# Performance work log

Measured on AMD Instinct MI355X. Metric: run time of the kernel, lower is better.

Reference implementation:

```python
import jax, jax.numpy as jnp
import numpy as np

TREE_DEPTH = 3
N_LEAVES = 2 ** TREE_DEPTH
TEMPERATURE = 1.0
N_HEADS = 16
SOFTPLUS_SHIFT = 0.5413


def _build_path_indices(n_leaves, tree_depth):
    pi = np.zeros((n_leaves, tree_depth), dtype=np.int32)
    pd = np.zeros((n_leaves, tree_depth), dtype=np.float32)
    for leaf in range(n_leaves):
        node = 0
        for d in range(tree_depth):
            pi[leaf, d] = node
            bit = (leaf >> (tree_depth - 1 - d)) & 1
            pd[leaf, d] = 1.0 - bit
            node = 2 * node + 1 + bit
    return pi, pd

PATH_IDX, PATH_DIR = _build_path_indices(N_LEAVES, TREE_DEPTH)


def setup_inputs() -> dict:
    key = jax.random.key(0)
    ks = jax.random.split(key, 8)
    B, S, D = 4, 1024, 1024
    T, N, L, H = 12, 7, 8, 3
    return {
        "x": jax.random.normal(ks[0], (B, S, D), jnp.float32),
        "decision_weights": jax.random.normal(ks[1], (T, N, D), jnp.float32) * 0.1,
        "decision_biases": jnp.zeros((T, N), jnp.float32),
        "node_temperature_logits": jnp.zeros((T, N), jnp.float32),
        "gate_w": jax.random.normal(ks[2], (D, T), jnp.float32) * (1.0 / np.sqrt(D)),
        "gate_b": jnp.zeros((T,), jnp.float32),
        "leaf_outputs": jax.random.normal(ks[3], (H, T, L, D), jnp.float32) * np.sqrt(2.0 / (L + D)),
        "out_w": jax.random.normal(ks[4], (D, D), jnp.float32) * (1.0 / np.sqrt(D)),
        "out_b": jnp.zeros((D,), jnp.float32),
    }


def _forest_qkv(x, dw, db, ntl, gate_w, gate_b, leaf_out):
    # routing: [B,S,T,n_internal]
    decisions = jnp.einsum('bsd,tnd->bstn', x, dw) + db
    node_temps = TEMPERATURE * jax.nn.softplus(ntl + SOFTPLUS_SHIFT)
    decisions = jax.nn.sigmoid(decisions / node_temps)
    # gather nodes along each root-to-leaf path: [B,S,T,L,depth]
    relevant = decisions[..., PATH_IDX]
    probs_per_level = PATH_DIR * relevant + (1.0 - PATH_DIR) * (1.0 - relevant)
    leaf_probs = jnp.prod(probs_per_level, axis=-1)  # [B,S,T,L]
    weights = jax.nn.softmax(x @ gate_w + gate_b, axis=-1)  # [B,S,T]
    # fused per-tree mix + gate combine (same math as per_tree->outputs)
    qkv = jnp.einsum('bstl,bst,htld->hbsd', leaf_probs, weights, leaf_out)
    return qkv[0], qkv[1], qkv[2]


def reference(x, decision_weights, decision_biases, node_temperature_logits,
              gate_w, gate_b, leaf_outputs, out_w, out_b):
    B, S, D = x.shape
    dh = D // N_HEADS
    q, k, v = _forest_qkv(x, decision_weights, decision_biases,
                          node_temperature_logits, gate_w, gate_b, leaf_outputs)
    q = q.reshape(B, S, N_HEADS, dh)
    k = k.reshape(B, S, N_HEADS, dh)
    v = v.reshape(B, S, N_HEADS, dh)
    scale = 1.0 / np.sqrt(dh)
    scores = jnp.einsum('bqhd,bkhd->bhqk', q, k) * scale
    causal = np.tril(np.ones((S, S), dtype=bool))
    scores = jnp.where(causal, scores, jnp.float32(-1e9))
    attn = jax.nn.softmax(scores, axis=-1)
    ctx = jnp.einsum('bhqk,bkhd->bqhd', attn, v).reshape(B, S, D)
    return ctx @ out_w + out_b
```

## Files before the change

kernel.cpp:

```cpp
#include <hip/hip_runtime.h>
#include <hip/hip_bf16.h>
#include <math.h>

#define TOKS 4096

typedef __attribute__((ext_vector_type(4))) float    f32x4;
typedef __attribute__((ext_vector_type(8))) short    short8;
typedef __attribute__((ext_vector_type(4))) unsigned short ushort4v;
typedef unsigned short ushort;

__device__ __forceinline__ ushort f2b(float f) {
    unsigned int b = __float_as_uint(f);
    b += 0x7fff + ((b >> 16) & 1);
    return (ushort)(b >> 16);
}

__global__ __launch_bounds__(256) void wb_kernel(
    const float* __restrict__ dw,
    const float* __restrict__ gate_w,
    ushort* __restrict__ Wb)
{
    const int i = blockIdx.x * 256 + threadIdx.x;
    const int row = i >> 7, k0 = (i & 127) * 8;
    short8 o;
    if (row < 84) {
        float4 a0 = *(const float4*)&dw[(size_t)row*1024 + k0];
        float4 a1 = *(const float4*)&dw[(size_t)row*1024 + k0 + 4];
        o[0]=(short)f2b(a0.x); o[1]=(short)f2b(a0.y); o[2]=(short)f2b(a0.z); o[3]=(short)f2b(a0.w);
        o[4]=(short)f2b(a1.x); o[5]=(short)f2b(a1.y); o[6]=(short)f2b(a1.z); o[7]=(short)f2b(a1.w);
    } else {
        const int t = row - 84;
        #pragma unroll
        for (int j = 0; j < 8; ++j) o[j] = (short)f2b(gate_w[(size_t)(k0+j)*12 + t]);
    }
    *(short8*)&Wb[(size_t)row*1024 + k0] = o;
}

__global__ __launch_bounds__(64) void route2_kernel(
    const float* __restrict__ x,
    const ushort* __restrict__ Wb,
    const float* __restrict__ db,
    const float* __restrict__ ntl,
    const float* __restrict__ gate_b,
    ushort* __restrict__ coeffb)
{
    const int tok0 = blockIdx.x * 16;
    const int lane = threadIdx.x;
    const int lq = lane & 15, lg = lane >> 4;
    __shared__ float lgt[16][97];

    f32x4 acc[6];
    #pragma unroll
    for (int n = 0; n < 6; ++n) acc[n] = (f32x4){0.f,0.f,0.f,0.f};

    for (int k0 = 0; k0 < 1024; k0 += 32) {
        float4 a0 = *(const float4*)&x[(size_t)(tok0 + lq)*1024 + k0 + lg*8];
        float4 a1 = *(const float4*)&x[(size_t)(tok0 + lq)*1024 + k0 + lg*8 + 4];
        short8 af;
        af[0]=(short)f2b(a0.x); af[1]=(short)f2b(a0.y); af[2]=(short)f2b(a0.z); af[3]=(short)f2b(a0.w);
        af[4]=(short)f2b(a1.x); af[5]=(short)f2b(a1.y); af[6]=(short)f2b(a1.z); af[7]=(short)f2b(a1.w);
        #pragma unroll
        for (int n = 0; n < 6; ++n) {
            short8 bf_ = *(const short8*)&Wb[(size_t)(n*16 + lq)*1024 + k0 + lg*8];
            acc[n] = __builtin_amdgcn_mfma_f32_16x16x32_bf16(af, bf_, acc[n], 0, 0, 0);
        }
    }

    #pragma unroll
    for (int n = 0; n < 6; ++n)
        #pragma unroll
        for (int r = 0; r < 4; ++r)
            lgt[lg*4 + r][n*16 + lq] = acc[n][r];
    __builtin_amdgcn_wave_barrier();

    const int tok = lane >> 2;
    #pragma unroll
    for (int tj = 0; tj < 3; ++tj) {
        const int t = (lane & 3)*3 + tj;
        float dec[7];
        #pragma unroll
        for (int n = 0; n < 7; ++n) {
            float tempv = log1pf(expf(ntl[t*7+n] + 0.5413f));
            float v = (lgt[tok][t*7+n] + db[t*7+n]) / tempv;
            dec[n] = 1.f / (1.f + expf(-v));
        }
        float g[12], gmax = -3e38f;
        #pragma unroll
        for (int tt = 0; tt < 12; ++tt) {
            g[tt] = lgt[tok][84+tt] + gate_b[tt];
            gmax = fmaxf(gmax, g[tt]);
        }
        float gsum = 0.f;
        #pragma unroll
        for (int tt = 0; tt < 12; ++tt) gsum += expf(g[tt]-gmax);
        const float wgt = expf(g[t]-gmax) / gsum;
        short8 co;
        #pragma unroll
        for (int l = 0; l < 8; ++l) {
            float p = wgt; int node = 0;
            #pragma unroll
            for (int dpt = 0; dpt < 3; ++dpt) {
                int bit = (l >> (2-dpt)) & 1;
                float r = dec[node];
                p *= bit ? (1.f - r) : r;
                node = 2*node + 1 + bit;
            }
            co[l] = (short)f2b(p);
        }
        *(short8*)&coeffb[(size_t)(tok0 + tok)*96 + t*8] = co;
    }
}

__global__ __launch_bounds__(256) void lt_kernel(
    const float* __restrict__ leaf, ushort* __restrict__ leafT)
{
    __shared__ float t[96][65];
    const int d0 = blockIdx.x * 64, h = blockIdx.y;
    const int tid = threadIdx.x;
    for (int i = tid; i < 96*16; i += 256) {
        int k = i >> 4, c4 = i & 15;
        *(float4*)&t[k][c4*4] = *(const float4*)&leaf[(size_t)(h*96 + k)*1024 + d0 + c4*4];
    }
    __syncthreads();
    const int d = tid >> 2, kq = (tid & 3) * 24;
    #pragma unroll
    for (int base = 0; base < 24; base += 8) {
        short8 o;
        #pragma unroll
        for (int j = 0; j < 8; ++j) o[j] = (short)f2b(t[kq+base+j][d]);
        *(short8*)&leafT[(size_t)(h*1024 + d0 + d)*96 + kq + base] = o;
    }
}

__global__ __launch_bounds__(256) void mix_kernel(
    const ushort* __restrict__ coeffb,
    const ushort* __restrict__ leafT,
    ushort* __restrict__ qkvb,
    ushort* __restrict__ vT)
{
    const int bt = blockIdx.x;
    const int bd = blockIdx.y;
    const int tid = threadIdx.x, w = tid >> 6, lane = tid & 63;
    const int lq = lane & 15, lg = lane >> 4;
    const int tok0 = bt*64 + w*16;
    const int c0 = bd*128;
    const int pl = c0 >> 10;
    const int d0 = c0 & 1023;

    f32x4 acc[8];
    #pragma unroll
    for (int n = 0; n < 8; ++n) acc[n] = (f32x4){0.f,0.f,0.f,0.f};

    #pragma unroll
    for (int ks = 0; ks < 3; ++ks) {
        const int k0 = ks*32;
        short8 bfrag = *(const short8*)&coeffb[(tok0 + lq)*96 + k0 + lg*8];
        #pragma unroll
        for (int n = 0; n < 8; ++n) {
            short8 afrag = *(const short8*)&leafT[(size_t)(pl*1024 + d0 + n*16 + lq)*96 + k0 + lg*8];
            acc[n] = __builtin_amdgcn_mfma_f32_16x16x32_bf16(afrag, bfrag, acc[n], 0, 0, 0);
        }
    }

    const int tok = tok0 + lq;
    if (pl < 2) {
        #pragma unroll
        for (int n = 0; n < 8; ++n) {
            const int d = d0 + n*16 + lg*4;
            ushort4v u;
            u[0]=f2b(acc[n][0]); u[1]=f2b(acc[n][1]);
            u[2]=f2b(acc[n][2]); u[3]=f2b(acc[n][3]);
            *(ushort4v*)&qkvb[(size_t)pl*TOKS*1024 + (size_t)tok*1024 + d] = u;
        }
    } else {
        const int b = tok >> 10, seq = tok & 1023;
        #pragma unroll
        for (int n = 0; n < 8; ++n) {
            #pragma unroll
            for (int r = 0; r < 4; ++r) {
                const int d = d0 + n*16 + lg*4 + r;
                const int head = d >> 6, dh = d & 63;
                vT[((size_t)((b*16+head)*64 + dh))*1024 + seq] = f2b(acc[n][r]);
            }
        }
    }
}

__global__ __launch_bounds__(256) void wtrans_kernel(
    const float* __restrict__ w, ushort* __restrict__ wT)
{
    __shared__ float t[64][65];
    const int n0 = blockIdx.x * 64, k0 = blockIdx.y * 64;
    const int tid = threadIdx.x;
    const int r = tid >> 2, c16 = (tid & 3) * 16;
    #pragma unroll
    for (int j = 0; j < 16; j += 4)
        *(float4*)&t[r][c16+j] = *(const float4*)&w[(size_t)(k0+r)*1024 + n0 + c16 + j];
    __syncthreads();
    short8 o0, o1;
    #pragma unroll
    for (int j = 0; j < 8; ++j) o0[j] = (short)f2b(t[c16+j][r]);
    #pragma unroll
    for (int j = 0; j < 8; ++j) o1[j] = (short)f2b(t[c16+8+j][r]);
    *(short8*)&wT[(size_t)(n0+r)*1024 + k0 + c16]     = o0;
    *(short8*)&wT[(size_t)(n0+r)*1024 + k0 + c16 + 8] = o1;
}

__global__ __launch_bounds__(64) void attn_kernel(
    const ushort* __restrict__ qk,
    const ushort* __restrict__ vT,
    ushort* __restrict__ ctxb)
{
    const int id = blockIdx.x;
    const int bh = id & 63;
    const int qt = 63 - (id >> 6);
    const int b = bh >> 4, h = bh & 15;
    const int lane = threadIdx.x;
    const int lq = lane & 15, lg = lane >> 4;
    __shared__ unsigned int pTu[128][13];

    const size_t plane = (size_t)TOKS*1024;
    const int tokq = b*1024 + qt*16 + lq;
    short8 aq[2];
    aq[0] = *(const short8*)&qk[(size_t)tokq*1024 + h*64 + lg*8];
    aq[1] = *(const short8*)&qk[(size_t)tokq*1024 + h*64 + 32 + lg*8];

    f32x4 o[4];
    #pragma unroll
    for (int n = 0; n < 4; ++n) o[n] = (f32x4){0.f,0.f,0.f,0.f};
    float m[4] = {-3e38f,-3e38f,-3e38f,-3e38f};
    float l[4] = {0.f,0.f,0.f,0.f};

    const ushort* Kp  = qk + plane;
    const ushort* vTp = vT + (size_t)bh*64*1024;
    const int nt = (qt >> 3) + 1;

    for (int t = 0; t < nt; ++t) {
        const int tk0 = b*1024 + t*128;
        f32x4 s[8];
        #pragma unroll
        for (int n = 0; n < 8; ++n) s[n] = (f32x4){0.f,0.f,0.f,0.f};
        #pragma unroll
        for (int kk = 0; kk < 2; ++kk)
            #pragma unroll
            for (int n = 0; n < 8; ++n) {
                short8 bk = *(const short8*)&Kp[(size_t)(tk0 + n*16 + lq)*1024 + h*64 + kk*32 + lg*8];
                s[n] = __builtin_amdgcn_mfma_f32_16x16x32_bf16(aq[kk], bk, s[n], 0, 0, 0);
            }

        const bool diag = (t == nt-1);
        if (diag) {
            #pragma unroll
            for (int n = 0; n < 8; ++n)
                #pragma unroll
                for (int r = 0; r < 4; ++r) {
                    float v = s[n][r] * 0.125f;
                    if (t*128 + n*16 + lq > qt*16 + lg*4 + r) v = -1e9f;
                    s[n][r] = v;
                }
        } else {
            #pragma unroll
            for (int n = 0; n < 8; ++n)
                #pragma unroll
                for (int r = 0; r < 4; ++r) s[n][r] *= 0.125f;
        }

        #pragma unroll
        for (int r = 0; r < 4; ++r) {
            float rm = fmaxf(fmaxf(fmaxf(s[0][r], s[1][r]), fmaxf(s[2][r], s[3][r])),
                             fmaxf(fmaxf(s[4][r], s[5][r]), fmaxf(s[6][r], s[7][r])));
            rm = fmaxf(rm, __shfl_xor(rm, 1));
            rm = fmaxf(rm, __shfl_xor(rm, 2));
            rm = fmaxf(rm, __shfl_xor(rm, 4));
            rm = fmaxf(rm, __shfl_xor(rm, 8));
            float mnew = fmaxf(m[r], rm);
            float corr = __expf(m[r] - mnew);
            float ps = 0.f;
            #pragma unroll
            for (int n = 0; n < 8; ++n) {
                float p = __expf(s[n][r] - mnew);
                s[n][r] = p; ps += p;
            }
            ps += __shfl_xor(ps, 1);
            ps += __shfl_xor(ps, 2);
            ps += __shfl_xor(ps, 4);
            ps += __shfl_xor(ps, 8);
            l[r] = l[r]*corr + ps;
            m[r] = mnew;
            o[0][r] *= corr; o[1][r] *= corr; o[2][r] *= corr; o[3][r] *= corr;
        }

        #pragma unroll
        for (int n = 0; n < 8; ++n) {
            unsigned int lo = (unsigned int)f2b(s[n][0]) | ((unsigned int)f2b(s[n][1]) << 16);
            unsigned int hi = (unsigned int)f2b(s[n][2]) | ((unsigned int)f2b(s[n][3]) << 16);
            pTu[n*16 + lq][lg*2]     = lo;
            pTu[n*16 + lq][lg*2 + 1] = hi;
        }
        __builtin_amdgcn_wave_barrier();

        short8 pa[4];
        #pragma unroll
        for (int kk = 0; kk < 4; ++kk)
            #pragma unroll
            for (int j = 0; j < 8; ++j) {
                unsigned int u = pTu[kk*32 + lg*8 + j][lq >> 1];
                pa[kk][j] = (short)(ushort)(u >> ((lq & 1) * 16));
            }
        __builtin_amdgcn_wave_barrier();

        #pragma unroll
        for (int kk = 0; kk < 4; ++kk)
            #pragma unroll
            for (int n = 0; n < 4; ++n) {
                short8 bv = *(const short8*)&vTp[(size_t)(n*16 + lq)*1024 + t*128 + kk*32 + lg*8];
                o[n] = __builtin_amdgcn_mfma_f32_16x16x32_bf16(pa[kk], bv, o[n], 0, 0, 0);
            }
    }

    #pragma unroll
    for (int r = 0; r < 4; ++r) {
        float inv = 1.f / l[r];
        int row = b*1024 + qt*16 + lg*4 + r;
        #pragma unroll
        for (int n = 0; n < 4; ++n)
            ctxb[(size_t)row*1024 + h*64 + n*16 + lq] = f2b(o[n][r] * inv);
    }
}

__global__ __launch_bounds__(256) void proj_kernel(
    const ushort* __restrict__ A,
    const ushort* __restrict__ Bt,
    const float* __restrict__ bias,
    float* __restrict__ out)
{
    const int bn = blockIdx.x, bm = blockIdx.y;
    const int tid = threadIdx.x, w = tid >> 6, lane = tid & 63;
    const int wm = w >> 1, wn = w & 1;
    const int lq = lane & 15, lg = lane >> 4;
    const int row0 = bm*128 + wm*64;
    const int col0 = bn*64 + wn*32;

    f32x4 acc[4][2];
    #pragma unroll
    for (int i = 0; i < 4; ++i)
        #pragma unroll
        for (int j = 0; j < 2; ++j) acc[i][j] = (f32x4){0.f,0.f,0.f,0.f};

    for (int k0 = 0; k0 < 1024; k0 += 32) {
        short8 a[4], bfr[2];
        #pragma unroll
        for (int i = 0; i < 4; ++i)
            a[i] = *(const short8*)&A[(size_t)(row0 + i*16 + lq)*1024 + k0 + lg*8];
        #pragma unroll
        for (int j = 0; j < 2; ++j)
            bfr[j] = *(const short8*)&Bt[(size_t)(col0 + j*16 + lq)*1024 + k0 + lg*8];
        #pragma unroll
        for (int i = 0; i < 4; ++i)
            #pragma unroll
            for (int j = 0; j < 2; ++j)
                acc[i][j] = __builtin_amdgcn_mfma_f32_16x16x32_bf16(a[i], bfr[j], acc[i][j], 0, 0, 0);
    }

    #pragma unroll
    for (int i = 0; i < 4; ++i)
        #pragma unroll
        for (int j = 0; j < 2; ++j) {
            int col = col0 + j*16 + lq;
            float bb = bias[col];
            #pragma unroll
            for (int r = 0; r < 4; ++r)
                out[(size_t)(row0 + i*16 + lg*4 + r)*1024 + col] = acc[i][j][r] + bb;
        }
}

extern "C" void kernel_launch(void* const* d_in, const int* in_sizes, int n_in,
                              void* d_out, int out_size, void* d_ws, size_t ws_size,
                              hipStream_t stream) {
    (void)in_sizes; (void)n_in; (void)out_size; (void)ws_size;
    const float* x      = (const float*)d_in[0];
    const float* dw     = (const float*)d_in[1];
    const float* db     = (const float*)d_in[2];
    const float* ntl    = (const float*)d_in[3];
    const float* gate_w = (const float*)d_in[4];
    const float* gate_b = (const float*)d_in[5];
    const float* leaf   = (const float*)d_in[6];
    const float* out_w  = (const float*)d_in[7];
    const float* out_b  = (const float*)d_in[8];
    float* out = (float*)d_out;

    ushort* coeffb = (ushort*)d_ws;
    ushort* Wb     = (ushort*)((char*)d_ws + ((size_t)1u  << 20));
    ushort* qkvb   = (ushort*)((char*)d_ws + ((size_t)2u  << 20));
    ushort* vT     = (ushort*)((char*)d_ws + ((size_t)20u << 20));
    ushort* ctxb   = (ushort*)((char*)d_ws + ((size_t)30u << 20));
    ushort* wT     = (ushort*)((char*)d_ws + ((size_t)40u << 20));
    ushort* leafT  = (ushort*)((char*)d_ws + ((size_t)44u << 20));

    hipLaunchKernelGGL(wb_kernel,      dim3(48),      dim3(256), 0, stream,
                       dw, gate_w, Wb);
    hipLaunchKernelGGL(lt_kernel,      dim3(16, 3),   dim3(256), 0, stream,
                       leaf, leafT);
    hipLaunchKernelGGL(wtrans_kernel,  dim3(16, 16),  dim3(256), 0, stream,
                       out_w, wT);
    hipLaunchKernelGGL(route2_kernel,  dim3(256),     dim3(64),  0, stream,
                       x, Wb, db, ntl, gate_b, coeffb);
    hipLaunchKernelGGL(mix_kernel,     dim3(64, 24),  dim3(256), 0, stream,
                       coeffb, leafT, qkvb, vT);
    hipLaunchKernelGGL(attn_kernel,    dim3(4096),    dim3(64),  0, stream,
                       qkvb, vT, ctxb);
    hipLaunchKernelGGL(proj_kernel,    dim3(16, 32),  dim3(256), 0, stream,
                       ctxb, wT, out_b, out);
}
```

Measured before the change: 290.0 us.

## Split routing GEMM K dimension across eight waves with shared-memory reduction

```diff
diff --git a/kernel.cpp b/kernel.cpp
--- a/kernel.cpp
+++ b/kernel.cpp
@@ -36,7 +36,7 @@
     *(short8*)&Wb[(size_t)row*1024 + k0] = o;
 }
 
-__global__ __launch_bounds__(64) void route2_kernel(
+__global__ __launch_bounds__(512) void route3_kernel(
     const float* __restrict__ x,
     const ushort* __restrict__ Wb,
     const float* __restrict__ db,
@@ -45,15 +45,20 @@
     ushort* __restrict__ coeffb)
 {
     const int tok0 = blockIdx.x * 16;
-    const int lane = threadIdx.x;
+    const int tid  = threadIdx.x;
+    const int wv   = tid >> 6;
+    const int lane = tid & 63;
     const int lq = lane & 15, lg = lane >> 4;
-    __shared__ float lgt[16][97];
+    __shared__ float part[8][16][100];
 
     f32x4 acc[6];
     #pragma unroll
     for (int n = 0; n < 6; ++n) acc[n] = (f32x4){0.f,0.f,0.f,0.f};
 
-    for (int k0 = 0; k0 < 1024; k0 += 32) {
+    const int kbase = wv * 128;
+    #pragma unroll
+    for (int ks = 0; ks < 4; ++ks) {
+        const int k0 = kbase + ks*32;
         float4 a0 = *(const float4*)&x[(size_t)(tok0 + lq)*1024 + k0 + lg*8];
         float4 a1 = *(const float4*)&x[(size_t)(tok0 + lq)*1024 + k0 + lg*8 + 4];
         short8 af;
@@ -70,24 +75,31 @@
     for (int n = 0; n < 6; ++n)
         #pragma unroll
         for (int r = 0; r < 4; ++r)
-            lgt[lg*4 + r][n*16 + lq] = acc[n][r];
-    __builtin_amdgcn_wave_barrier();
-
-    const int tok = lane >> 2;
-    #pragma unroll
-    for (int tj = 0; tj < 3; ++tj) {
-        const int t = (lane & 3)*3 + tj;
+            part[wv][lg*4 + r][n*16 + lq] = acc[n][r];
+    __syncthreads();
+
+    for (int i = tid; i < 1536; i += 512) {
+        const int tk = i / 96, c = i - tk*96;
+        float s = part[0][tk][c];
+        #pragma unroll
+        for (int w = 1; w < 8; ++w) s += part[w][tk][c];
+        part[0][tk][c] = s;
+    }
+    __syncthreads();
+
+    if (tid < 192) {
+        const int lt = tid / 12, t = tid - lt*12;
         float dec[7];
         #pragma unroll
         for (int n = 0; n < 7; ++n) {
             float tempv = log1pf(expf(ntl[t*7+n] + 0.5413f));
-            float v = (lgt[tok][t*7+n] + db[t*7+n]) / tempv;
+            float v = (part[0][lt][t*7+n] + db[t*7+n]) / tempv;
             dec[n] = 1.f / (1.f + expf(-v));
         }
         float g[12], gmax = -3e38f;
         #pragma unroll
         for (int tt = 0; tt < 12; ++tt) {
-            g[tt] = lgt[tok][84+tt] + gate_b[tt];
+            g[tt] = part[0][lt][84+tt] + gate_b[tt];
             gmax = fmaxf(gmax, g[tt]);
         }
         float gsum = 0.f;
@@ -107,7 +119,7 @@
             }
             co[l] = (short)f2b(p);
         }
-        *(short8*)&coeffb[(size_t)(tok0 + tok)*96 + t*8] = co;
+        *(short8*)&coeffb[(size_t)(tok0 + lt)*96 + t*8] = co;
     }
 }
 
@@ -403,7 +415,7 @@
                        leaf, leafT);
     hipLaunchKernelGGL(wtrans_kernel,  dim3(16, 16),  dim3(256), 0, stream,
                        out_w, wT);
-    hipLaunchKernelGGL(route2_kernel,  dim3(256),     dim3(64),  0, stream,
+    hipLaunchKernelGGL(route3_kernel,  dim3(256),     dim3(512), 0, stream,
                        x, Wb, db, ntl, gate_b, coeffb);
     hipLaunchKernelGGL(mix_kernel,     dim3(64, 24),  dim3(256), 0, stream,
                        coeffb, leafT, qkvb, vT);
```

After: 244.6 us. 15.6% less time.
